# Kernel tuning notes

Hardware: AMD Instinct MI355X
Metric: run time of the kernel (lower is better)

## Reference

```python
import jax, jax.numpy as jnp
import numpy as np

N = 100000  # nodes
E = 1600000  # edges

def gcn_layer(x, W, b, src, tgt, ew):
    # support = x @ W + b ; messages gathered at src, weighted scatter-sum into tgt
    h = x @ W + b                      # [N, F_out]
    msg = h[src] * ew[:, None]         # [E, F_out]
    return jax.ops.segment_sum(msg, tgt, num_segments=N)  # [N, F_out]

def setup_inputs() -> dict:
    key = jax.random.key(0)
    ks = jax.random.split(key, 12)
    nfeat, nhid, nclass = 256, 128, 40
    x = jax.random.normal(ks[0], (N, nfeat), dtype=jnp.float32)
    src = jax.random.randint(ks[1], (E,), 0, N)
    tgt = jax.random.randint(ks[2], (E,), 0, N)
    edge_weight = jax.random.uniform(ks[3], (E,), dtype=jnp.float32)
    def w(k, fi, fo):
        return jax.random.normal(k, (fi, fo), dtype=jnp.float32) / np.sqrt(fi)
    return {
        "x": x, "src": src, "tgt": tgt, "edge_weight": edge_weight,
        "W0": w(ks[4], nfeat, nhid), "b0": jnp.zeros((nhid,), jnp.float32),
        "W1": w(ks[5], nhid, nhid),  "b1": jnp.zeros((nhid,), jnp.float32),
        "W2": w(ks[6], nhid, nhid),  "b2": jnp.zeros((nhid,), jnp.float32),
        "W3": w(ks[7], nhid, nclass),"b3": jnp.zeros((nclass,), jnp.float32),
    }

def reference(x, src, tgt, edge_weight, W0, b0, W1, b1, W2, b2, W3, b3):
    # RESK2 with nlayers=4, eval mode (dropout = identity).
    # x0 = relu(gc0); r = x0; x1 = relu(gc1); x2 = relu(gc2) + r; out = log_softmax(gc3)
    x0 = jax.nn.relu(gcn_layer(x, W0, b0, src, tgt, edge_weight))
    r = x0
    x1 = jax.nn.relu(gcn_layer(x0, W1, b1, src, tgt, edge_weight))
    x2 = jax.nn.relu(gcn_layer(x1, W2, b2, src, tgt, edge_weight)) + r
    logits = gcn_layer(x2, W3, b3, src, tgt, edge_weight)
    return jax.nn.log_softmax(logits, axis=1)
```

## Files before the change

### kernel.cpp

```cpp
#include <hip/hip_runtime.h>
#include <hip/hip_bf16.h>


typedef __attribute__((ext_vector_type(8))) short short8;
typedef __attribute__((ext_vector_type(4))) float float4v;

#define SC_SHIFT 8
#define SC_NODES 256
#define FILL_CAP 12288
#define SRC_MASK 0x1FFFF

static __device__ __forceinline__ float bf2f_lo(unsigned int v) {
    return __uint_as_float(v << 16);
}
static __device__ __forceinline__ float bf2f_hi(unsigned int v) {
    return __uint_as_float(v & 0xffff0000u);
}
static __device__ __forceinline__ unsigned short f2bf(float f) {
    unsigned int u = __float_as_uint(f);
    u = (u + 0x7fffu + ((u >> 16) & 1u)) >> 16;
    return (unsigned short)u;
}
static __device__ __forceinline__ unsigned int packbf(float a, float b) {
    return (unsigned int)f2bf(a) | ((unsigned int)f2bf(b) << 16);
}
static __device__ __forceinline__ float pw_w(unsigned int pe) {
    return __uint_as_float((pe >> 17) << 16);
}

static __device__ __forceinline__ void acc8(float* acc, uint4 v, float wt) {
    acc[0] = fmaf(bf2f_lo(v.x), wt, acc[0]);
    acc[1] = fmaf(bf2f_hi(v.x), wt, acc[1]);
    acc[2] = fmaf(bf2f_lo(v.y), wt, acc[2]);
    acc[3] = fmaf(bf2f_hi(v.y), wt, acc[3]);
    acc[4] = fmaf(bf2f_lo(v.z), wt, acc[4]);
    acc[5] = fmaf(bf2f_hi(v.z), wt, acc[5]);
    acc[6] = fmaf(bf2f_lo(v.w), wt, acc[6]);
    acc[7] = fmaf(bf2f_hi(v.w), wt, acc[7]);
}
static __device__ __forceinline__ void acc4(float* acc, uint2 v, float wt) {
    acc[0] = fmaf(bf2f_lo(v.x), wt, acc[0]);
    acc[1] = fmaf(bf2f_hi(v.x), wt, acc[1]);
    acc[2] = fmaf(bf2f_lo(v.y), wt, acc[2]);
    acc[3] = fmaf(bf2f_hi(v.y), wt, acc[3]);
}

__global__ __launch_bounds__(256) void k_count(const int* __restrict__ tgt,
                                               int* __restrict__ chunkTot,
                                               int E, int NSC) {
    __shared__ int hist[512];
    const int tid = threadIdx.x;
    hist[tid] = 0;
    hist[tid + 256] = 0;
    __syncthreads();
#pragma unroll
    for (int r = 0; r < 4; r++) {
        int e = blockIdx.x * 4096 + r * 1024 + tid * 4;
        if (e + 3 < E) {
            int4 tv = *(const int4*)&tgt[e];
            atomicAdd(&hist[tv.x >> SC_SHIFT], 1);
            atomicAdd(&hist[tv.y >> SC_SHIFT], 1);
            atomicAdd(&hist[tv.z >> SC_SHIFT], 1);
            atomicAdd(&hist[tv.w >> SC_SHIFT], 1);
        } else {
            for (int j = 0; j < 4; j++)
                if (e + j < E) atomicAdd(&hist[tgt[e + j] >> SC_SHIFT], 1);
        }
    }
    __syncthreads();
    for (int i = tid; i < NSC; i += 256) {
        int c = hist[i];
        if (c) atomicAdd(&chunkTot[i], c);
    }
}

__global__ __launch_bounds__(512) void k_scanB(const int* __restrict__ chunkTot,
                                               int* __restrict__ chunkStart,
                                               int* __restrict__ chunkCur,
                                               int E, int NSC) {
    __shared__ int sm[512];
    const int tid = threadIdx.x;
    int v = (tid < NSC) ? chunkTot[tid] : 0;
    sm[tid] = v;
    __syncthreads();
    for (int off = 1; off < 512; off <<= 1) {
        int t = (tid >= off) ? sm[tid - off] : 0;
        __syncthreads();
        sm[tid] += t;
        __syncthreads();
    }
    int excl = sm[tid] - v;
    if (tid < NSC) {
        chunkStart[tid] = excl;
        chunkCur[tid * 32] = excl;
    }
    if (tid == 0) chunkStart[NSC] = E;
}

__global__ __launch_bounds__(512) void k_bucket(const int* __restrict__ src,
                                                const int* __restrict__ tgt,
                                                const float* __restrict__ ew,
                                                int* __restrict__ chunkCur,
                                                unsigned int* __restrict__ st_pw,
                                                unsigned char* __restrict__ st_t8,
                                                int E) {
    __shared__ int cnt[512];
    __shared__ int rk[512];
    __shared__ int bbase[512];
    const int tid = threadIdx.x;
    cnt[tid] = 0;
    rk[tid] = 0;
    __syncthreads();

    int t16[16];
    unsigned int p16[16];
#pragma unroll
    for (int r = 0; r < 4; r++) {
        int e = blockIdx.x * 8192 + r * 2048 + tid * 4;
        if (e + 3 < E) {
            int4 tv = *(const int4*)&tgt[e];
            int4 sv = *(const int4*)&src[e];
            float4 wv = *(const float4*)&ew[e];
            t16[r * 4 + 0] = tv.x; t16[r * 4 + 1] = tv.y;
            t16[r * 4 + 2] = tv.z; t16[r * 4 + 3] = tv.w;
            p16[r * 4 + 0] = ((unsigned int)f2bf(wv.x) << 17) | (unsigned int)sv.x;
            p16[r * 4 + 1] = ((unsigned int)f2bf(wv.y) << 17) | (unsigned int)sv.y;
            p16[r * 4 + 2] = ((unsigned int)f2bf(wv.z) << 17) | (unsigned int)sv.z;
            p16[r * 4 + 3] = ((unsigned int)f2bf(wv.w) << 17) | (unsigned int)sv.w;
        } else {
            for (int j = 0; j < 4; j++) {
                int ee = e + j;
                t16[r * 4 + j] = (ee < E) ? tgt[ee] : -1;
                p16[r * 4 + j] = (ee < E)
                    ? (((unsigned int)f2bf(ew[ee]) << 17) | (unsigned int)src[ee])
                    : 0u;
            }
        }
    }
#pragma unroll
    for (int j = 0; j < 16; j++)
        if (t16[j] >= 0) atomicAdd(&cnt[t16[j] >> SC_SHIFT], 1);
    __syncthreads();
    {
        int c = cnt[tid];
        bbase[tid] = c ? atomicAdd(&chunkCur[tid * 32], c) : 0;
    }
    __syncthreads();
#pragma unroll
    for (int j = 0; j < 16; j++) {
        if (t16[j] >= 0) {
            int c = t16[j] >> SC_SHIFT;
            int pos = bbase[c] + atomicAdd(&rk[c], 1);
            st_pw[pos] = p16[j];
            st_t8[pos] = (unsigned char)(t16[j] & (SC_NODES - 1));
        }
    }
}

__global__ __launch_bounds__(256) void k_fill2(const unsigned int* __restrict__ st_pw,
                                               const unsigned char* __restrict__ st_t8,
                                               const int* __restrict__ chunkStart,
                                               int* __restrict__ rowptr,
                                               unsigned int* __restrict__ perm,
                                               int N, int E, int NSC) {
    __shared__ int lhist[SC_NODES];
    __shared__ int lcur[SC_NODES];
    __shared__ unsigned int ledge[FILL_CAP];
    const int tid = threadIdx.x;
    const int b = blockIdx.x;
    const int n0 = b << SC_SHIFT;
    const int nlocal = min(SC_NODES, N - n0);
    const int sstart = chunkStart[b];
    const int send = chunkStart[b + 1];
    const int cnt = send - sstart;

    lhist[tid] = 0;
    __syncthreads();
    for (int e = sstart + tid; e < send; e += 256)
        atomicAdd(&lhist[st_t8[e]], 1);
    __syncthreads();
    int v = lhist[tid];
    __syncthreads();
    lhist[tid] = v;
    __syncthreads();
    for (int off = 1; off < 256; off <<= 1) {
        int t = (tid >= off) ? lhist[tid - off] : 0;
        __syncthreads();
        lhist[tid] += t;
        __syncthreads();
    }
    int excl = lhist[tid] - v;
    if (tid < nlocal) rowptr[n0 + tid] = sstart + excl;
    if (b == NSC - 1 && tid == 0) rowptr[N] = E;
    lcur[tid] = excl;
    __syncthreads();

    if (cnt <= FILL_CAP) {
        for (int e = sstart + tid; e < send; e += 256) {
            int lt = st_t8[e];
            int pos = atomicAdd(&lcur[lt], 1);
            ledge[pos] = st_pw[e];
        }
        __syncthreads();
        for (int i = tid; i < cnt; i += 256) perm[sstart + i] = ledge[i];
    } else {
        for (int e = sstart + tid; e < send; e += 256) {
            int lt = st_t8[e];
            int pos = atomicAdd(&lcur[lt], 1);
            perm[sstart + pos] = st_pw[e];
        }
    }
}

__global__ __launch_bounds__(256) void k_wtrans_all(
    const float* __restrict__ W0, const float* __restrict__ W1,
    const float* __restrict__ W2, const float* __restrict__ W3,
    unsigned short* __restrict__ Wt0, unsigned short* __restrict__ Wt1,
    unsigned short* __restrict__ Wt2, unsigned short* __restrict__ Wt3,
    int* __restrict__ chunkTot) {
    int idx = blockIdx.x * 256 + threadIdx.x;
    if (idx < 512) chunkTot[idx] = 0;
    if (idx < 32768) {
        int c = idx >> 8, k = idx & 255;
        Wt0[idx] = f2bf(W0[k * 128 + c]);
    } else if (idx < 49152) {
        int i = idx - 32768;
        int c = i >> 7, k = i & 127;
        Wt1[i] = f2bf(W1[k * 128 + c]);
    } else if (idx < 65536) {
        int i = idx - 49152;
        int c = i >> 7, k = i & 127;
        Wt2[i] = f2bf(W2[k * 128 + c]);
    } else if (idx < 71680) {
        int i = idx - 65536;
        int c = i >> 7, k = i & 127;
        Wt3[i] = (c < 40) ? f2bf(W3[k * 40 + c]) : 0;
    }
}

template <int K, int AF32>
__global__ __launch_bounds__(256) void k_gemm_mfma(const void* __restrict__ Av,
                                                   const unsigned short* __restrict__ Wt,
                                                   const float* __restrict__ bias,
                                                   unsigned short* __restrict__ C, int N) {
    __shared__ unsigned short As[128 * 40];
    __shared__ unsigned short Bs[128 * 40];
    const unsigned short* A16 = (const unsigned short*)Av;
    const float* A32 = (const float*)Av;
    const int tid = threadIdx.x;
    const int wave = tid >> 6, lane = tid & 63;
    const int quad = lane >> 4, l15 = lane & 15;
    const int rowBase = blockIdx.x * 128;

    const float4v z = {0.f, 0.f, 0.f, 0.f};
    float4v acc[2][8];
#pragma unroll
    for (int i = 0; i < 2; i++)
#pragma unroll
        for (int j = 0; j < 8; j++) acc[i][j] = z;

    for (int k0 = 0; k0 < K; k0 += 32) {
#pragma unroll
        for (int i = 0; i < 2; i++) {
            int t = i * 256 + tid;
            int r = t >> 2;
            int kc = t & 3;
            int rg = rowBase + r;
            rg = rg < N ? rg : N - 1;
            uint4 va;
            if (AF32) {
                float4 f0 = *(const float4*)&A32[(size_t)rg * K + k0 + kc * 8];
                float4 f1 = *(const float4*)&A32[(size_t)rg * K + k0 + kc * 8 + 4];
                va.x = packbf(f0.x, f0.y);
                va.y = packbf(f0.z, f0.w);
                va.z = packbf(f1.x, f1.y);
                va.w = packbf(f1.z, f1.w);
            } else {
                va = *(const uint4*)&A16[(size_t)rg * K + k0 + kc * 8];
            }
            *(uint4*)&As[r * 40 + kc * 8] = va;
            uint4 vb = *(const uint4*)&Wt[(size_t)r * K + k0 + kc * 8];
            *(uint4*)&Bs[r * 40 + kc * 8] = vb;
        }
        __syncthreads();

        short8 a0 = *(const short8*)&As[(wave * 32 + l15) * 40 + quad * 8];
        short8 a1 = *(const short8*)&As[(wave * 32 + 16 + l15) * 40 + quad * 8];
#pragma unroll
        for (int c = 0; c < 8; c++) {
            short8 b = *(const short8*)&Bs[(c * 16 + l15) * 40 + quad * 8];
            acc[0][c] = __builtin_amdgcn_mfma_f32_16x16x32_bf16(a0, b, acc[0][c], 0, 0, 0);
            acc[1][c] = __builtin_amdgcn_mfma_f32_16x16x32_bf16(a1, b, acc[1][c], 0, 0, 0);
        }
        __syncthreads();
    }

#pragma unroll
    for (int rt = 0; rt < 2; rt++) {
#pragma unroll
        for (int c = 0; c < 8; c++) {
            int col = c * 16 + l15;
            float bv = bias[col];
#pragma unroll
            for (int i = 0; i < 4; i++) {
                int row = rowBase + wave * 32 + rt * 16 + quad * 4 + i;
                if (row < N) C[(size_t)row * 128 + col] = f2bf(acc[rt][c][i] + bv);
            }
        }
    }
}

__global__ __launch_bounds__(256) void k_gemm40_mfma(const unsigned short* __restrict__ A,
                                                     const unsigned short* __restrict__ Wt3,
                                                     const float* __restrict__ bias,
                                                     unsigned short* __restrict__ C, int N) {
    __shared__ unsigned short As[128 * 40];
    __shared__ unsigned short Bs[48 * 136];
    const int tid = threadIdx.x;
    const int wave = tid >> 6, lane = tid & 63;
    const int quad = lane >> 4, l15 = lane & 15;
    const int rowBase = blockIdx.x * 128;

    for (int t = tid; t < 48 * 16; t += 256) {
        int r = t >> 4, kc = t & 15;
        uint4 v = *(const uint4*)&Wt3[r * 128 + kc * 8];
        *(uint4*)&Bs[r * 136 + kc * 8] = v;
    }

    const float4v z = {0.f, 0.f, 0.f, 0.f};
    float4v acc[2][3];
#pragma unroll
    for (int i = 0; i < 2; i++)
#pragma unroll
        for (int j = 0; j < 3; j++) acc[i][j] = z;

    for (int k0 = 0; k0 < 128; k0 += 32) {
#pragma unroll
        for (int i = 0; i < 2; i++) {
            int t = i * 256 + tid;
            int r = t >> 2;
            int kc = t & 3;
            int rg = rowBase + r;
            rg = rg < N ? rg : N - 1;
            uint4 va = *(const uint4*)&A[(size_t)rg * 128 + k0 + kc * 8];
            *(uint4*)&As[r * 40 + kc * 8] = va;
        }
        __syncthreads();

        short8 a0 = *(const short8*)&As[(wave * 32 + l15) * 40 + quad * 8];
        short8 a1 = *(const short8*)&As[(wave * 32 + 16 + l15) * 40 + quad * 8];
#pragma unroll
        for (int c = 0; c < 3; c++) {
            short8 b = *(const short8*)&Bs[(c * 16 + l15) * 136 + k0 + quad * 8];
            acc[0][c] = __builtin_amdgcn_mfma_f32_16x16x32_bf16(a0, b, acc[0][c], 0, 0, 0);
            acc[1][c] = __builtin_amdgcn_mfma_f32_16x16x32_bf16(a1, b, acc[1][c], 0, 0, 0);
        }
        __syncthreads();
    }

#pragma unroll
    for (int rt = 0; rt < 2; rt++) {
#pragma unroll
        for (int c = 0; c < 3; c++) {
            int col = c * 16 + l15;
            if (col < 40) {
                float bv = bias[col];
#pragma unroll
                for (int i = 0; i < 4; i++) {
                    int row = rowBase + wave * 32 + rt * 16 + quad * 4 + i;
                    if (row < N) C[(size_t)row * 64 + col] = f2bf(acc[rt][c][i] + bv);
                }
            }
        }
    }
}

__global__ __launch_bounds__(256) void k_agg128(const unsigned short* __restrict__ h,
                                                const int* __restrict__ rowptr,
                                                const unsigned int* __restrict__ perm,
                                                const unsigned short* __restrict__ resid,
                                                unsigned short* __restrict__ out, int N) {
    int node = (blockIdx.x * 256 + threadIdx.x) >> 6;
    if (node >= N) return;
    const int lane = threadIdx.x & 63;
    const int g = lane >> 4, l = lane & 15;
    const int beg = rowptr[node], end = rowptr[node + 1];
    const int last = end - 1;

    float acc[8] = {};
    for (int base = beg; base < end; base += 16) {
        int e0 = base + g, e1 = base + 4 + g, e2 = base + 8 + g, e3 = base + 12 + g;
        unsigned int p0 = perm[e0 <= last ? e0 : last];
        unsigned int p1 = perm[e1 <= last ? e1 : last];
        unsigned int p2 = perm[e2 <= last ? e2 : last];
        unsigned int p3 = perm[e3 <= last ? e3 : last];
        uint4 a0 = *(const uint4*)&h[(size_t)(p0 & SRC_MASK) * 128 + l * 8];
        uint4 a1 = *(const uint4*)&h[(size_t)(p1 & SRC_MASK) * 128 + l * 8];
        uint4 a2 = *(const uint4*)&h[(size_t)(p2 & SRC_MASK) * 128 + l * 8];
        uint4 a3 = *(const uint4*)&h[(size_t)(p3 & SRC_MASK) * 128 + l * 8];
        float w0 = e0 <= last ? pw_w(p0) : 0.f;
        float w1 = e1 <= last ? pw_w(p1) : 0.f;
        float w2 = e2 <= last ? pw_w(p2) : 0.f;
        float w3 = e3 <= last ? pw_w(p3) : 0.f;
        acc8(acc, a0, w0);
        acc8(acc, a1, w1);
        acc8(acc, a2, w2);
        acc8(acc, a3, w3);
    }

#pragma unroll
    for (int i = 0; i < 8; i++) {
        acc[i] += __shfl_xor(acc[i], 16);
        acc[i] += __shfl_xor(acc[i], 32);
    }

    if (g == 0) {
#pragma unroll
        for (int i = 0; i < 8; i++) acc[i] = fmaxf(acc[i], 0.f);
        if (resid) {
            uint4 rv = *(const uint4*)&resid[(size_t)node * 128 + l * 8];
            acc[0] += bf2f_lo(rv.x); acc[1] += bf2f_hi(rv.x);
            acc[2] += bf2f_lo(rv.y); acc[3] += bf2f_hi(rv.y);
            acc[4] += bf2f_lo(rv.z); acc[5] += bf2f_hi(rv.z);
            acc[6] += bf2f_lo(rv.w); acc[7] += bf2f_hi(rv.w);
        }
        uint4 o;
        o.x = packbf(acc[0], acc[1]);
        o.y = packbf(acc[2], acc[3]);
        o.z = packbf(acc[4], acc[5]);
        o.w = packbf(acc[6], acc[7]);
        *(uint4*)&out[(size_t)node * 128 + l * 8] = o;
    }
}

__global__ __launch_bounds__(256) void k_agg40_lsm(const unsigned short* __restrict__ h,
                                                   const int* __restrict__ rowptr,
                                                   const unsigned int* __restrict__ perm,
                                                   float* __restrict__ out, int N) {
    int node = (blockIdx.x * 256 + threadIdx.x) >> 6;
    if (node >= N) return;
    const int lane = threadIdx.x & 63;
    const int g = lane >> 4, l = lane & 15;
    const int beg = rowptr[node], end = rowptr[node + 1];
    const int last = end - 1;
    const int lc = l < 10 ? l : 0;

    float acc[4] = {};
    for (int base = beg; base < end; base += 16) {
        int e0 = base + g, e1 = base + 4 + g, e2 = base + 8 + g, e3 = base + 12 + g;
        unsigned int p0 = perm[e0 <= last ? e0 : last];
        unsigned int p1 = perm[e1 <= last ? e1 : last];
        unsigned int p2 = perm[e2 <= last ? e2 : last];
        unsigned int p3 = perm[e3 <= last ? e3 : last];
        uint2 a0 = *(const uint2*)&h[(size_t)(p0 & SRC_MASK) * 64 + lc * 4];
        uint2 a1 = *(const uint2*)&h[(size_t)(p1 & SRC_MASK) * 64 + lc * 4];
        uint2 a2 = *(const uint2*)&h[(size_t)(p2 & SRC_MASK) * 64 + lc * 4];
        uint2 a3 = *(const uint2*)&h[(size_t)(p3 & SRC_MASK) * 64 + lc * 4];
        float w0 = e0 <= last ? pw_w(p0) : 0.f;
        float w1 = e1 <= last ? pw_w(p1) : 0.f;
        float w2 = e2 <= last ? pw_w(p2) : 0.f;
        float w3 = e3 <= last ? pw_w(p3) : 0.f;
        acc4(acc, a0, w0);
        acc4(acc, a1, w1);
        acc4(acc, a2, w2);
        acc4(acc, a3, w3);
    }
#pragma unroll
    for (int i = 0; i < 4; i++) {
        acc[i] += __shfl_xor(acc[i], 16);
        acc[i] += __shfl_xor(acc[i], 32);
    }

    bool vf = l < 10;
    float m = vf ? fmaxf(fmaxf(acc[0], acc[1]), fmaxf(acc[2], acc[3]))
                 : -__builtin_inff();
#pragma unroll
    for (int off = 1; off < 16; off <<= 1) m = fmaxf(m, __shfl_xor(m, off));
    float s = vf ? (expf(acc[0] - m) + expf(acc[1] - m) +
                    expf(acc[2] - m) + expf(acc[3] - m))
                 : 0.f;
#pragma unroll
    for (int off = 1; off < 16; off <<= 1) s += __shfl_xor(s, off);
    float ls = m + logf(s);
    if (g == 0 && vf) {
        float4 o = make_float4(acc[0] - ls, acc[1] - ls, acc[2] - ls, acc[3] - ls);
        *(float4*)&out[(size_t)node * 40 + l * 4] = o;
    }
}

extern "C" void kernel_launch(void* const* d_in, const int* in_sizes, int n_in,
                              void* d_out, int out_size, void* d_ws, size_t ws_size,
                              hipStream_t stream) {
    const float* x  = (const float*)d_in[0];
    const int*   src = (const int*)d_in[1];
    const int*   tgt = (const int*)d_in[2];
    const float* ew  = (const float*)d_in[3];
    const float* W0 = (const float*)d_in[4];
    const float* b0 = (const float*)d_in[5];
    const float* W1 = (const float*)d_in[6];
    const float* b1 = (const float*)d_in[7];
    const float* W2 = (const float*)d_in[8];
    const float* b2 = (const float*)d_in[9];
    const float* W3 = (const float*)d_in[10];
    const float* b3 = (const float*)d_in[11];

    const int N = in_sizes[0] / 256;
    const int E = in_sizes[1];
    const int NSC = (N + SC_NODES - 1) >> SC_SHIFT;

    char* ws = (char*)d_ws;
    size_t off = 0;
    auto alloc = [&](size_t bytes) -> void* {
        void* p = ws + off;
        off = (off + bytes + 255) & ~(size_t)255;
        return p;
    };
    unsigned short* XCb = (unsigned short*)alloc((size_t)N * 128 * 2);
    size_t hbytes = (size_t)N * 128 * 2;
    size_t sbytes = (size_t)E * 5 + 256;
    char* hbuf = (char*)alloc(hbytes > sbytes ? hbytes : sbytes);
    unsigned short* Hb = (unsigned short*)hbuf;
    unsigned int* st_pw = (unsigned int*)hbuf;
    unsigned char* st_t8 = (unsigned char*)(hbuf + (size_t)E * 4);
    char* buf1 = (char*)alloc((size_t)N * 128 * 2);
    unsigned short* XAb  = (unsigned short*)buf1;
    unsigned short* H40b = (unsigned short*)buf1;
    unsigned short* XBb  = (unsigned short*)alloc((size_t)N * 128 * 2);
    int*   rowptr    = (int*)alloc((size_t)(N + 1) * 4);
    int*   chunkTot  = (int*)alloc(512 * 4);
    int*   chunkStart= (int*)alloc(520 * 4);
    int*   chunkCur  = (int*)alloc(512 * 32 * 4);
    unsigned int* perm = (unsigned int*)alloc((size_t)E * 4);
    unsigned short* Wt0 = (unsigned short*)alloc(256 * 128 * 2);
    unsigned short* Wt1 = (unsigned short*)alloc(128 * 128 * 2);
    unsigned short* Wt2 = (unsigned short*)alloc(128 * 128 * 2);
    unsigned short* Wt3 = (unsigned short*)alloc(48 * 128 * 2);
    (void)ws_size;

    float* logits = (float*)d_out;

    k_wtrans_all<<<(71680 + 255) / 256, 256, 0, stream>>>(W0, W1, W2, W3,
                                                          Wt0, Wt1, Wt2, Wt3,
                                                          chunkTot);
    k_count<<<(E + 4095) / 4096, 256, 0, stream>>>(tgt, chunkTot, E, NSC);
    k_scanB<<<1, 512, 0, stream>>>(chunkTot, chunkStart, chunkCur, E, NSC);
    k_bucket<<<(E + 8191) / 8192, 512, 0, stream>>>(src, tgt, ew, chunkCur,
                                                    st_pw, st_t8, E);
    k_fill2<<<NSC, 256, 0, stream>>>(st_pw, st_t8, chunkStart, rowptr, perm,
                                     N, E, NSC);

    const int gGemm = (N + 127) / 128;
    const int gWave = (N + 3) / 4;

    k_gemm_mfma<256, 1><<<gGemm, 256, 0, stream>>>(x, Wt0, b0, Hb, N);
    k_agg128<<<gWave, 256, 0, stream>>>(Hb, rowptr, perm, nullptr, XAb, N);
    k_gemm_mfma<128, 0><<<gGemm, 256, 0, stream>>>(XAb, Wt1, b1, Hb, N);
    k_agg128<<<gWave, 256, 0, stream>>>(Hb, rowptr, perm, nullptr, XBb, N);
    k_gemm_mfma<128, 0><<<gGemm, 256, 0, stream>>>(XBb, Wt2, b2, Hb, N);
    k_agg128<<<gWave, 256, 0, stream>>>(Hb, rowptr, perm, XAb, XCb, N);
    k_gemm40_mfma<<<gGemm, 256, 0, stream>>>(XCb, Wt3, b3, H40b, N);
    k_agg40_lsm<<<gWave, 256, 0, stream>>>(H40b, rowptr, perm, logits, N);
}
```

Before: 518.0 us.

## Register-prefetch GEMM tiles and vectorize transposed MFMA epilogue stores

```diff
diff --git a/kernel.cpp b/kernel.cpp
--- a/kernel.cpp
+++ b/kernel.cpp
@@ -245,6 +245,7 @@
                                                    unsigned short* __restrict__ C, int N) {
     __shared__ unsigned short As[128 * 40];
     __shared__ unsigned short Bs[128 * 40];
+    __shared__ float bsh[128];
     const unsigned short* A16 = (const unsigned short*)Av;
     const float* A32 = (const float*)Av;
     const int tid = threadIdx.x;
@@ -252,6 +253,32 @@
     const int quad = lane >> 4, l15 = lane & 15;
     const int rowBase = blockIdx.x * 128;
 
+    if (tid < 128) bsh[tid] = bias[tid];
+
+    const int r0 = tid >> 2, kc0 = tid & 3;
+    const int r1 = (256 + tid) >> 2, kc1 = kc0;
+    int rg0 = rowBase + r0; rg0 = rg0 < N ? rg0 : N - 1;
+    int rg1 = rowBase + r1; rg1 = rg1 < N ? rg1 : N - 1;
+
+    uint4 pa[2], pb[2];
+    auto load_step = [&](int k0) {
+        if (AF32) {
+            float4 f0 = *(const float4*)&A32[(size_t)rg0 * K + k0 + kc0 * 8];
+            float4 f1 = *(const float4*)&A32[(size_t)rg0 * K + k0 + kc0 * 8 + 4];
+            pa[0].x = packbf(f0.x, f0.y); pa[0].y = packbf(f0.z, f0.w);
+            pa[0].z = packbf(f1.x, f1.y); pa[0].w = packbf(f1.z, f1.w);
+            float4 g0 = *(const float4*)&A32[(size_t)rg1 * K + k0 + kc1 * 8];
+            float4 g1 = *(const float4*)&A32[(size_t)rg1 * K + k0 + kc1 * 8 + 4];
+            pa[1].x = packbf(g0.x, g0.y); pa[1].y = packbf(g0.z, g0.w);
+            pa[1].z = packbf(g1.x, g1.y); pa[1].w = packbf(g1.z, g1.w);
+        } else {
+            pa[0] = *(const uint4*)&A16[(size_t)rg0 * K + k0 + kc0 * 8];
+            pa[1] = *(const uint4*)&A16[(size_t)rg1 * K + k0 + kc1 * 8];
+        }
+        pb[0] = *(const uint4*)&Wt[(size_t)r0 * K + k0 + kc0 * 8];
+        pb[1] = *(const uint4*)&Wt[(size_t)r1 * K + k0 + kc1 * 8];
+    };
+
     const float4v z = {0.f, 0.f, 0.f, 0.f};
     float4v acc[2][8];
 #pragma unroll
@@ -259,52 +286,38 @@
 #pragma unroll
         for (int j = 0; j < 8; j++) acc[i][j] = z;
 
+    load_step(0);
     for (int k0 = 0; k0 < K; k0 += 32) {
-#pragma unroll
-        for (int i = 0; i < 2; i++) {
-            int t = i * 256 + tid;
-            int r = t >> 2;
-            int kc = t & 3;
-            int rg = rowBase + r;
-            rg = rg < N ? rg : N - 1;
-            uint4 va;
-            if (AF32) {
-                float4 f0 = *(const float4*)&A32[(size_t)rg * K + k0 + kc * 8];
-                float4 f1 = *(const float4*)&A32[(size_t)rg * K + k0 + kc * 8 + 4];
-                va.x = packbf(f0.x, f0.y);
-                va.y = packbf(f0.z, f0.w);
-                va.z = packbf(f1.x, f1.y);
-                va.w = packbf(f1.z, f1.w);
-            } else {
-                va = *(const uint4*)&A16[(size_t)rg * K + k0 + kc * 8];
-            }
-            *(uint4*)&As[r * 40 + kc * 8] = va;
-            uint4 vb = *(const uint4*)&Wt[(size_t)r * K + k0 + kc * 8];
-            *(uint4*)&Bs[r * 40 + kc * 8] = vb;
-        }
-        __syncthreads();
+        *(uint4*)&As[r0 * 40 + kc0 * 8] = pa[0];
+        *(uint4*)&As[r1 * 40 + kc1 * 8] = pa[1];
+        *(uint4*)&Bs[r0 * 40 + kc0 * 8] = pb[0];
+        *(uint4*)&Bs[r1 * 40 + kc1 * 8] = pb[1];
+        __syncthreads();
+        if (k0 + 32 < K) load_step(k0 + 32);
 
         short8 a0 = *(const short8*)&As[(wave * 32 + l15) * 40 + quad * 8];
         short8 a1 = *(const short8*)&As[(wave * 32 + 16 + l15) * 40 + quad * 8];
 #pragma unroll
         for (int c = 0; c < 8; c++) {
             short8 b = *(const short8*)&Bs[(c * 16 + l15) * 40 + quad * 8];
-            acc[0][c] = __builtin_amdgcn_mfma_f32_16x16x32_bf16(a0, b, acc[0][c], 0, 0, 0);
-            acc[1][c] = __builtin_amdgcn_mfma_f32_16x16x32_bf16(a1, b, acc[1][c], 0, 0, 0);
+            acc[0][c] = __builtin_amdgcn_mfma_f32_16x16x32_bf16(b, a0, acc[0][c], 0, 0, 0);
+            acc[1][c] = __builtin_amdgcn_mfma_f32_16x16x32_bf16(b, a1, acc[1][c], 0, 0, 0);
         }
         __syncthreads();
     }
 
 #pragma unroll
     for (int rt = 0; rt < 2; rt++) {
-#pragma unroll
-        for (int c = 0; c < 8; c++) {
-            int col = c * 16 + l15;
-            float bv = bias[col];
-#pragma unroll
-            for (int i = 0; i < 4; i++) {
-                int row = rowBase + wave * 32 + rt * 16 + quad * 4 + i;
-                if (row < N) C[(size_t)row * 128 + col] = f2bf(acc[rt][c][i] + bv);
+        int row = rowBase + wave * 32 + rt * 16 + l15;
+        if (row < N) {
+#pragma unroll
+            for (int c = 0; c < 8; c++) {
+                int colBase = c * 16 + quad * 4;
+                float4 bv = *(const float4*)&bsh[colBase];
+                uint2 o;
+                o.x = packbf(acc[rt][c][0] + bv.x, acc[rt][c][1] + bv.y);
+                o.y = packbf(acc[rt][c][2] + bv.z, acc[rt][c][3] + bv.w);
+                *(uint2*)&C[(size_t)row * 128 + colBase] = o;
             }
         }
     }
@@ -316,17 +329,30 @@
                                                      unsigned short* __restrict__ C, int N) {
     __shared__ unsigned short As[128 * 40];
     __shared__ unsigned short Bs[48 * 136];
+    __shared__ float bsh[48];
     const int tid = threadIdx.x;
     const int wave = tid >> 6, lane = tid & 63;
     const int quad = lane >> 4, l15 = lane & 15;
     const int rowBase = blockIdx.x * 128;
 
+    if (tid < 48) bsh[tid] = (tid < 40) ? bias[tid] : 0.f;
     for (int t = tid; t < 48 * 16; t += 256) {
         int r = t >> 4, kc = t & 15;
         uint4 v = *(const uint4*)&Wt3[r * 128 + kc * 8];
         *(uint4*)&Bs[r * 136 + kc * 8] = v;
     }
 
+    const int r0 = tid >> 2, kc0 = tid & 3;
+    const int r1 = r0 + 64;
+    int rg0 = rowBase + r0; rg0 = rg0 < N ? rg0 : N - 1;
+    int rg1 = rowBase + r1; rg1 = rg1 < N ? rg1 : N - 1;
+
+    uint4 pa[2];
+    auto load_step = [&](int k0) {
+        pa[0] = *(const uint4*)&A[(size_t)rg0 * 128 + k0 + kc0 * 8];
+        pa[1] = *(const uint4*)&A[(size_t)rg1 * 128 + k0 + kc0 * 8];
+    };
+
     const float4v z = {0.f, 0.f, 0.f, 0.f};
     float4v acc[2][3];
 #pragma unroll
@@ -334,42 +360,36 @@
 #pragma unroll
         for (int j = 0; j < 3; j++) acc[i][j] = z;
 
+    load_step(0);
     for (int k0 = 0; k0 < 128; k0 += 32) {
-#pragma unroll
-        for (int i = 0; i < 2; i++) {
-            int t = i * 256 + tid;
-            int r = t >> 2;
-            int kc = t & 3;
-            int rg = rowBase + r;
-            rg = rg < N ? rg : N - 1;
-            uint4 va = *(const uint4*)&A[(size_t)rg * 128 + k0 + kc * 8];
-            *(uint4*)&As[r * 40 + kc * 8] = va;
-        }
-        __syncthreads();
+        *(uint4*)&As[r0 * 40 + kc0 * 8] = pa[0];
+        *(uint4*)&As[r1 * 40 + kc0 * 8] = pa[1];
+        __syncthreads();
+        if (k0 + 32 < 128) load_step(k0 + 32);
 
         short8 a0 = *(const short8*)&As[(wave * 32 + l15) * 40 + quad * 8];
         short8 a1 = *(const short8*)&As[(wave * 32 + 16 + l15) * 40 + quad * 8];
 #pragma unroll
         for (int c = 0; c < 3; c++) {
             short8 b = *(const short8*)&Bs[(c * 16 + l15) * 136 + k0 + quad * 8];
-            acc[0][c] = __builtin_amdgcn_mfma_f32_16x16x32_bf16(a0, b, acc[0][c], 0, 0, 0);
-            acc[1][c] = __builtin_amdgcn_mfma_f32_16x16x32_bf16(a1, b, acc[1][c], 0, 0, 0);
+            acc[0][c] = __builtin_amdgcn_mfma_f32_16x16x32_bf16(b, a0, acc[0][c], 0, 0, 0);
+            acc[1][c] = __builtin_amdgcn_mfma_f32_16x16x32_bf16(b, a1, acc[1][c], 0, 0, 0);
         }
         __syncthreads();
     }
 
 #pragma unroll
     for (int rt = 0; rt < 2; rt++) {
-#pragma unroll
-        for (int c = 0; c < 3; c++) {
-            int col = c * 16 + l15;
-            if (col < 40) {
-                float bv = bias[col];
-#pragma unroll
-                for (int i = 0; i < 4; i++) {
-                    int row = rowBase + wave * 32 + rt * 16 + quad * 4 + i;
-                    if (row < N) C[(size_t)row * 64 + col] = f2bf(acc[rt][c][i] + bv);
-                }
+        int row = rowBase + wave * 32 + rt * 16 + l15;
+        if (row < N) {
+#pragma unroll
+            for (int c = 0; c < 3; c++) {
+                int colBase = c * 16 + quad * 4;
+                float4 bv = *(const float4*)&bsh[colBase];
+                uint2 o;
+                o.x = packbf(acc[rt][c][0] + bv.x, acc[rt][c][1] + bv.y);
+                o.y = packbf(acc[rt][c][2] + bv.z, acc[rt][c][3] + bv.w);
+                *(uint2*)&C[(size_t)row * 64 + colBase] = o;
             }
         }
     }
```

Result: slower. 548.2 us (+5.8%).
